# Kernel optimization log

Measured on AMD Instinct MI355X. Metric: run time of the kernel, lower is better.

## Reference

```python
import jax, jax.numpy as jnp
import numpy as np

B, S, D, H = 4, 2048, 1024, 16
DK = D // H


def setup_inputs() -> dict:
    key = jax.random.key(0)
    ks = jax.random.split(key, 9)
    sc = 1.0 / np.sqrt(D)
    return {
        "query": jax.random.normal(ks[0], (B, S, D), jnp.float32),
        "key": jax.random.normal(ks[1], (B, S, D), jnp.float32),
        "value": jax.random.normal(ks[2], (B, S, D), jnp.float32),
        "Wq": jax.random.normal(ks[3], (D, D), jnp.float32) * sc,
        "bq": jax.random.normal(ks[4], (D,), jnp.float32) * sc,
        "Wk": jax.random.normal(ks[5], (D, D), jnp.float32) * sc,
        "bk": jax.random.normal(ks[6], (D,), jnp.float32) * sc,
        "Wv": jax.random.normal(ks[7], (D, D), jnp.float32) * sc,
        "bv": jax.random.normal(ks[8], (D,), jnp.float32) * sc,
    }


def reference(query, key, value, Wq, bq, Wk, bk, Wv, bv):
    # QKV projections, split into heads: [B,S,D] -> [B,H,S,DK]
    q = (query @ Wq + bq).reshape(B, S, H, DK).transpose(0, 2, 1, 3)
    k = (key @ Wk + bk).reshape(B, S, H, DK).transpose(0, 2, 1, 3)
    v = (value @ Wv + bv).reshape(B, S, H, DK).transpose(0, 2, 1, 3)
    # NOTE: original module applies NO 1/sqrt(d_k) scaling
    attn = jnp.einsum("bhqd,bhkd->bhqk", q, k)
    attn = jax.nn.softmax(attn, axis=-1)  # dropout is identity at inference
    ctx = jnp.einsum("bhqk,bhkd->bhqd", attn, v)
    ctx = ctx.transpose(0, 2, 1, 3).reshape(B, S, D)
    # original adds residual to raw concatenated context (no output projection)
    return ctx + query
```

## Files before the change

### kernel.cpp

```cpp
#include <hip/hip_runtime.h>
#include <hip/hip_bf16.h>
#include <stdint.h>

#define Bb 4
#define Ss 2048
#define Dd 1024
#define Hh 16
#define DK 64
#define BH 64
#define Mm 8192
#define KVT 64

typedef __attribute__((ext_vector_type(8))) _Float16 f16x8;
typedef __attribute__((ext_vector_type(2))) _Float16 f16x2;
typedef __attribute__((ext_vector_type(4))) float f32x4;
typedef __attribute__((ext_vector_type(16))) float f32x16;
typedef __attribute__((ext_vector_type(2))) unsigned uint2v;

__device__ __forceinline__ void gload16(const _Float16* g, _Float16* lds) {
  __builtin_amdgcn_global_load_lds((const __attribute__((address_space(1))) unsigned int*)g,
                                   (__attribute__((address_space(3))) unsigned int*)lds, 16, 0, 0);
}

__device__ __forceinline__ unsigned pk2(float a, float b) {
  union { f16x2 h; unsigned u; } x;
  x.h[0] = (_Float16)a; x.h[1] = (_Float16)b;
  return x.u;
}

__global__ __launch_bounds__(256) void cvt_act(const float* __restrict__ q,
                                               const float* __restrict__ k,
                                               const float* __restrict__ v,
                                               _Float16* __restrict__ xq,
                                               _Float16* __restrict__ xk,
                                               _Float16* __restrict__ xv) {
  const float* src = blockIdx.z == 0 ? q : (blockIdx.z == 1 ? k : v);
  _Float16* dst = blockIdx.z == 0 ? xq : (blockIdx.z == 1 ? xk : xv);
  int i = (blockIdx.x * 256 + threadIdx.x) * 8;
  float4 a = *(const float4*)(src + i);
  float4 b = *(const float4*)(src + i + 4);
  union { f16x8 v8; _Float16 h[8]; } o;
  o.h[0] = (_Float16)a.x; o.h[1] = (_Float16)a.y; o.h[2] = (_Float16)a.z; o.h[3] = (_Float16)a.w;
  o.h[4] = (_Float16)b.x; o.h[5] = (_Float16)b.y; o.h[6] = (_Float16)b.z; o.h[7] = (_Float16)b.w;
  *(f16x8*)(dst + i) = o.v8;
}

__global__ __launch_bounds__(256) void cvt_wt(const float* __restrict__ wq,
                                              const float* __restrict__ wk,
                                              const float* __restrict__ wv,
                                              _Float16* __restrict__ tq,
                                              _Float16* __restrict__ tk,
                                              _Float16* __restrict__ tv) {
  const float* w = blockIdx.z == 0 ? wq : (blockIdx.z == 1 ? wk : wv);
  _Float16* o = blockIdx.z == 0 ? tq : (blockIdx.z == 1 ? tk : tv);
  __shared__ float tile[64][65];
  int k0 = blockIdx.x * 64;
  int n0 = blockIdx.y * 64;
  int t = threadIdx.x;
  int tr = t >> 4;
  int tc = (t & 15) * 4;
  for (int i = 0; i < 4; i++) {
    int r = i * 16 + tr;
    float4 val = *(const float4*)(w + (k0 + r) * Dd + n0 + tc);
    tile[r][tc + 0] = val.x; tile[r][tc + 1] = val.y;
    tile[r][tc + 2] = val.z; tile[r][tc + 3] = val.w;
  }
  __syncthreads();
  for (int i = 0; i < 2; i++) {
    int vdx = t + 256 * i;
    int rn = vdx >> 3;
    int c8 = (vdx & 7) * 8;
    union { f16x8 v8; _Float16 h[8]; } o2;
    for (int j = 0; j < 8; j++) o2.h[j] = (_Float16)tile[c8 + j][rn];
    *(f16x8*)(o + (n0 + rn) * Dd + k0 + c8) = o2.v8;
  }
}

__global__ __launch_bounds__(256) void gemm_qkv(
    const _Float16* __restrict__ xq, const _Float16* __restrict__ xk,
    const _Float16* __restrict__ xv,
    const _Float16* __restrict__ wtq, const _Float16* __restrict__ wtk,
    const _Float16* __restrict__ wtv,
    const float* __restrict__ bq, const float* __restrict__ bk, const float* __restrict__ bv,
    _Float16* __restrict__ oq, _Float16* __restrict__ ok,
    _Float16* __restrict__ ov) {
  int z = blockIdx.z;
  const _Float16* A  = z == 0 ? xq  : (z == 1 ? xk  : xv);
  const _Float16* Bt = z == 0 ? wtq : (z == 1 ? wtk : wtv);
  const float* bias  = z == 0 ? bq  : (z == 1 ? bk  : bv);
  _Float16* out      = z == 0 ? oq  : (z == 1 ? ok  : ov);

  __shared__ _Float16 As[128 * 64];
  __shared__ _Float16 Bs[128 * 64];

  int tid = threadIdx.x;
  int w = tid >> 6;
  int l = tid & 63;
  int lr = l & 15, lk = l >> 4;
  int m0 = blockIdx.x * 128;
  int n0 = blockIdx.y * 128;
  int wr = (w >> 1) * 64;
  int wc = (w & 1) * 64;

  f32x4 acc[4][4] = {};

  for (int kt = 0; kt < Dd; kt += 64) {
    __syncthreads();
    for (int i = 0; i < 4; i++) {
      int fbase = i * 256 + w * 64;
      int f = fbase + l;
      int r = f >> 3, c = (f & 7) * 8;
      gload16(A + (m0 + r) * Dd + kt + c, &As[fbase * 8]);
      gload16(Bt + (n0 + r) * Dd + kt + c, &Bs[fbase * 8]);
    }
    __syncthreads();
    for (int kh = 0; kh < 2; kh++) {
      f16x8 af[4], bfr[4];
      for (int mi = 0; mi < 4; mi++)
        af[mi] = *(const f16x8*)&As[(wr + mi * 16 + lr) * 64 + kh * 32 + lk * 8];
      for (int ni = 0; ni < 4; ni++)
        bfr[ni] = *(const f16x8*)&Bs[(wc + ni * 16 + lr) * 64 + kh * 32 + lk * 8];
      for (int mi = 0; mi < 4; mi++)
        for (int ni = 0; ni < 4; ni++)
          acc[mi][ni] = __builtin_amdgcn_mfma_f32_16x16x32_f16(af[mi], bfr[ni], acc[mi][ni], 0, 0, 0);
    }
  }

  for (int mi = 0; mi < 4; mi++) {
    for (int ni = 0; ni < 4; ni++) {
      int n = n0 + wc + ni * 16 + lr;
      float bval = bias[n];
      int h = n >> 6, dk = n & 63;
      for (int j = 0; j < 4; j++) {
        int m = m0 + wr + mi * 16 + lk * 4 + j;
        int b = m >> 11, s = m & 2047;
        out[((b * Hh + h) * Ss + s) * DK + dk] = (_Float16)(acc[mi][ni][j] + bval);
      }
    }
  }
}

__global__ __launch_bounds__(256) void transpose_v(const unsigned short* __restrict__ vin,
                                                   unsigned short* __restrict__ vout) {
  __shared__ unsigned short t[64][80];
  typedef __attribute__((ext_vector_type(8))) short s16x8;
  int bh = blockIdx.y;
  int s0 = blockIdx.x * 64;
  int tid = threadIdx.x;
  const unsigned short* vp = vin + bh * (Ss * DK);
  for (int i = 0; i < 2; i++) {
    int v = tid + 256 * i;
    int r = v >> 3, c8 = (v & 7) * 8;
    s16x8 val = *(const s16x8*)(vp + (s0 + r) * DK + c8);
    *(s16x8*)&t[r][c8] = val;
  }
  __syncthreads();
  unsigned short* op = vout + bh * (DK * Ss);
  for (int i = 0; i < 2; i++) {
    int v = tid + 256 * i;
    int rn = v >> 3;
    int c8 = (v & 7) * 8;
    union { s16x8 v8; unsigned short u[8]; } o2;
    for (int j = 0; j < 8; j++) o2.u[j] = t[c8 + j][rn];
    *(s16x8*)(op + rn * Ss + s0 + c8) = o2.v8;
  }
}

__global__ __launch_bounds__(256) void attn(const _Float16* __restrict__ Qb,
                                            const _Float16* __restrict__ Kb,
                                            const _Float16* __restrict__ Vt,
                                            const float* __restrict__ query,
                                            float* __restrict__ outp) {
  __shared__ _Float16 Kl[2][KVT * 64];
  __shared__ _Float16 Vl[2][KVT * 64];

  int tid = threadIdx.x;
  int w = tid >> 6, l = tid & 63;
  int l31 = l & 31, hi = l >> 5;
  int bh = blockIdx.x;
  int q0 = blockIdx.y * 128 + w * 32;
  const _Float16* Qp = Qb + bh * (Ss * DK);
  const _Float16* Kp = Kb + bh * (Ss * DK);
  const _Float16* Vp = Vt + bh * (DK * Ss);

  int srow = l >> 3;
  int sslot = (l & 7) ^ (srow & 7);
  int w16 = w * 16;
  const _Float16* ksrc0 = Kp + (w16 + srow) * DK + sslot * 8;
  const _Float16* ksrc1 = Kp + (w16 + 8 + srow) * DK + sslot * 8;
  const _Float16* vsrc0 = Vp + (w16 + srow) * Ss + sslot * 8;
  const _Float16* vsrc1 = Vp + (w16 + 8 + srow) * Ss + sslot * 8;

#define STAGE(KV0, BUF)                                                   \
  {                                                                       \
    gload16(ksrc0 + (KV0) * DK, &Kl[BUF][w16 * 64]);                      \
    gload16(ksrc1 + (KV0) * DK, &Kl[BUF][(w16 + 8) * 64]);                \
    gload16(vsrc0 + (KV0), &Vl[BUF][w16 * 64]);                           \
    gload16(vsrc1 + (KV0), &Vl[BUF][(w16 + 8) * 64]);                     \
  }

  f16x8 qf[4];
#pragma unroll
  for (int s = 0; s < 4; s++)
    qf[s] = *(const f16x8*)(Qp + (q0 + l31) * DK + s * 16 + hi * 8);

  f32x16 o0 = {}, o1 = {};
  float mrun = -1e30f, lrun = 0.f;

  int kv7 = l31 & 7;
  int rslot[4];
#pragma unroll
  for (int s = 0; s < 4; s++) rslot[s] = ((s * 2 + hi) ^ kv7) * 8;

  STAGE(0, 0)
  __syncthreads();

  int cur = 0;
  for (int kv0 = 0; kv0 < Ss; kv0 += KVT) {
    if (kv0 + KVT < Ss) STAGE(kv0 + KVT, cur ^ 1)

    const _Float16* Kc = &Kl[cur][0];
    f32x16 s0 = {}, s1 = {};
#pragma unroll
    for (int s = 0; s < 4; s++) {
      f16x8 ka = *(const f16x8*)&Kc[l31 * 64 + rslot[s]];
      s0 = __builtin_amdgcn_mfma_f32_32x32x16_f16(ka, qf[s], s0, 0, 0, 0);
    }
#pragma unroll
    for (int s = 0; s < 4; s++) {
      f16x8 kb = *(const f16x8*)&Kc[(32 + l31) * 64 + rslot[s]];
      s1 = __builtin_amdgcn_mfma_f32_32x32x16_f16(kb, qf[s], s1, 0, 0, 0);
    }

    float m8[8];
#pragma unroll
    for (int r = 0; r < 8; r++)
      m8[r] = fmaxf(fmaxf(s0[r], s0[r + 8]), fmaxf(s1[r], s1[r + 8]));
#pragma unroll
    for (int d = 4; d >= 1; d >>= 1)
#pragma unroll
      for (int r = 0; r < 4; r++) if (r < d) m8[r] = fmaxf(m8[r], m8[r + d]);
    float pm = fmaxf(m8[0], __shfl_xor(m8[0], 32));

    if (!__all(pm - mrun <= 8.f)) {
      float mn = fmaxf(mrun, pm);
      float sc_ = __expf(mrun - mn);
      mrun = mn;
      lrun *= sc_;
#pragma unroll
      for (int r = 0; r < 16; r++) { o0[r] *= sc_; o1[r] *= sc_; }
    }
#pragma unroll
    for (int r = 0; r < 16; r++) {
      s0[r] = __expf(s0[r] - mrun);
      s1[r] = __expf(s1[r] - mrun);
    }
    float sm[8];
#pragma unroll
    for (int r = 0; r < 8; r++) sm[r] = (s0[r] + s0[r + 8]) + (s1[r] + s1[r + 8]);
#pragma unroll
    for (int d = 4; d >= 1; d >>= 1)
#pragma unroll
      for (int r = 0; r < 4; r++) if (r < d) sm[r] += sm[r + d];
    lrun += sm[0] + __shfl_xor(sm[0], 32);

    const _Float16* Vc = &Vl[cur][0];
#define PVSTEP(SRC, OFF, KST)                                                   \
    {                                                                           \
      unsigned a0 = pk2(SRC[(OFF) + 0], SRC[(OFF) + 1]);                        \
      unsigned a1 = pk2(SRC[(OFF) + 2], SRC[(OFF) + 3]);                        \
      unsigned b0 = pk2(SRC[(OFF) + 4], SRC[(OFF) + 5]);                        \
      unsigned b1 = pk2(SRC[(OFF) + 6], SRC[(OFF) + 7]);                        \
      uint2v r0 = __builtin_amdgcn_permlane32_swap(a0, b0, false, false);       \
      uint2v r1 = __builtin_amdgcn_permlane32_swap(a1, b1, false, false);       \
      union { unsigned u[4]; f16x8 v; } pf;                                     \
      pf.u[0] = r0[0]; pf.u[1] = r1[0]; pf.u[2] = r0[1]; pf.u[3] = r1[1];       \
      f16x8 v0 = *(const f16x8*)&Vc[l31 * 64 + rslot[KST]];                     \
      f16x8 v1 = *(const f16x8*)&Vc[(32 + l31) * 64 + rslot[KST]];              \
      o0 = __builtin_amdgcn_mfma_f32_32x32x16_f16(v0, pf.v, o0, 0, 0, 0);       \
      o1 = __builtin_amdgcn_mfma_f32_32x32x16_f16(v1, pf.v, o1, 0, 0, 0);       \
    }
    PVSTEP(s0, 0, 0)
    PVSTEP(s0, 8, 1)
    PVSTEP(s1, 0, 2)
    PVSTEP(s1, 8, 3)
#undef PVSTEP

    __syncthreads();
    cur ^= 1;
  }

  int b = bh >> 4, h = bh & 15;
  float inv = 1.f / lrun;
  int base = (b * Ss + q0 + l31) * Dd + h * 64;
#pragma unroll
  for (int rq = 0; rq < 4; rq++) {
    int d0 = rq * 8 + hi * 4;
    float4 qv0 = *(const float4*)(query + base + d0);
    float4 ov0;
    ov0.x = o0[rq * 4 + 0] * inv + qv0.x;
    ov0.y = o0[rq * 4 + 1] * inv + qv0.y;
    ov0.z = o0[rq * 4 + 2] * inv + qv0.z;
    ov0.w = o0[rq * 4 + 3] * inv + qv0.w;
    *(float4*)(outp + base + d0) = ov0;
    float4 qv1 = *(const float4*)(query + base + 32 + d0);
    float4 ov1;
    ov1.x = o1[rq * 4 + 0] * inv + qv1.x;
    ov1.y = o1[rq * 4 + 1] * inv + qv1.y;
    ov1.z = o1[rq * 4 + 2] * inv + qv1.z;
    ov1.w = o1[rq * 4 + 3] * inv + qv1.w;
    *(float4*)(outp + base + 32 + d0) = ov1;
  }
#undef STAGE
}

extern "C" void kernel_launch(void* const* d_in, const int* in_sizes, int n_in,
                              void* d_out, int out_size, void* d_ws, size_t ws_size,
                              hipStream_t stream) {
  const float* query = (const float*)d_in[0];
  const float* key   = (const float*)d_in[1];
  const float* value = (const float*)d_in[2];
  const float* Wq = (const float*)d_in[3];
  const float* bq = (const float*)d_in[4];
  const float* Wk = (const float*)d_in[5];
  const float* bk = (const float*)d_in[6];
  const float* Wv = (const float*)d_in[7];
  const float* bv = (const float*)d_in[8];
  float* out = (float*)d_out;

  _Float16* ws = (_Float16*)d_ws;
  const size_t ACT = (size_t)Mm * Dd;
  const size_t WSZ = (size_t)Dd * Dd;
  _Float16* Xq   = ws;
  _Float16* Xk   = Xq + ACT;
  _Float16* Xv   = Xk + ACT;
  _Float16* Wtq  = Xv + ACT;
  _Float16* Wtk  = Wtq + WSZ;
  _Float16* Wtv  = Wtk + WSZ;
  _Float16* Qb   = Wtv + WSZ;
  _Float16* Kb   = Qb + ACT;
  _Float16* Vtmp = Kb + ACT;
  _Float16* VtT  = Vtmp + ACT;

  cvt_act<<<dim3(4096, 1, 3), dim3(256), 0, stream>>>(query, key, value, Xq, Xk, Xv);
  cvt_wt<<<dim3(16, 16, 3), dim3(256), 0, stream>>>(Wq, Wk, Wv, Wtq, Wtk, Wtv);
  gemm_qkv<<<dim3(64, 8, 3), dim3(256), 0, stream>>>(Xq, Xk, Xv, Wtq, Wtk, Wtv,
                                                     bq, bk, bv, Qb, Kb, Vtmp);
  transpose_v<<<dim3(32, 64), dim3(256), 0, stream>>>((const unsigned short*)Vtmp,
                                                      (unsigned short*)VtT);
  attn<<<dim3(64, 16), dim3(256), 0, stream>>>(Qb, Kb, VtT, query, out);
}
```

Baseline: 234.5 us.

## Fuse V transpose into GEMM epilogue, fold log2e into Wq, use exp2

The GEMM epilogue for V now writes the transposed [bh, dk, s] layout directly with 4-wide stores, so the separate transpose kernel and its extra pass over V are gone. Wq and bq are pre-scaled by log2(e) so softmax can use exp2f instead of __expf. The per-tile cross-lane shuffle for the row sum is deferred to a single shuffle after the loop, fp16 packing uses cvt_pkrtz, and s_setprio is raised around the MFMA blocks. Scaling Wq in fp16 changes rounding slightly, and cvt_pkrtz rounds toward zero rather than to nearest.

```diff
diff --git a/kernel.cpp b/kernel.cpp
--- a/kernel.cpp
+++ b/kernel.cpp
@@ -12,7 +12,8 @@
 #define KVT 64
 
 typedef __attribute__((ext_vector_type(8))) _Float16 f16x8;
-typedef __attribute__((ext_vector_type(2))) _Float16 f16x2;
+typedef __attribute__((ext_vector_type(4))) _Float16 f16x4;
+typedef __attribute__((ext_vector_type(2))) __fp16 fp16x2;
 typedef __attribute__((ext_vector_type(4))) float f32x4;
 typedef __attribute__((ext_vector_type(16))) float f32x16;
 typedef __attribute__((ext_vector_type(2))) unsigned uint2v;
@@ -22,9 +23,9 @@
                                    (__attribute__((address_space(3))) unsigned int*)lds, 16, 0, 0);
 }
 
-__device__ __forceinline__ unsigned pk2(float a, float b) {
-  union { f16x2 h; unsigned u; } x;
-  x.h[0] = (_Float16)a; x.h[1] = (_Float16)b;
+__device__ __forceinline__ unsigned pk2u(float a, float b) {
+  union { fp16x2 h; unsigned u; } x;
+  x.h = __builtin_amdgcn_cvt_pkrtz(a, b);
   return x.u;
 }
 
@@ -53,6 +54,7 @@
                                               _Float16* __restrict__ tv) {
   const float* w = blockIdx.z == 0 ? wq : (blockIdx.z == 1 ? wk : wv);
   _Float16* o = blockIdx.z == 0 ? tq : (blockIdx.z == 1 ? tk : tv);
+  float wscale = blockIdx.z == 0 ? 1.4426950408889634f : 1.0f;
   __shared__ float tile[64][65];
   int k0 = blockIdx.x * 64;
   int n0 = blockIdx.y * 64;
@@ -71,7 +73,7 @@
     int rn = vdx >> 3;
     int c8 = (vdx & 7) * 8;
     union { f16x8 v8; _Float16 h[8]; } o2;
-    for (int j = 0; j < 8; j++) o2.h[j] = (_Float16)tile[c8 + j][rn];
+    for (int j = 0; j < 8; j++) o2.h[j] = (_Float16)(tile[c8 + j][rn] * wscale);
     *(f16x8*)(o + (n0 + rn) * Dd + k0 + c8) = o2.v8;
   }
 }
@@ -89,6 +91,7 @@
   const _Float16* Bt = z == 0 ? wtq : (z == 1 ? wtk : wtv);
   const float* bias  = z == 0 ? bq  : (z == 1 ? bk  : bv);
   _Float16* out      = z == 0 ? oq  : (z == 1 ? ok  : ov);
+  float bscale       = z == 0 ? 1.4426950408889634f : 1.0f;
 
   __shared__ _Float16 As[128 * 64];
   __shared__ _Float16 Bs[128 * 64];
@@ -126,43 +129,32 @@
     }
   }
 
-  for (int mi = 0; mi < 4; mi++) {
-    for (int ni = 0; ni < 4; ni++) {
-      int n = n0 + wc + ni * 16 + lr;
-      float bval = bias[n];
-      int h = n >> 6, dk = n & 63;
-      for (int j = 0; j < 4; j++) {
-        int m = m0 + wr + mi * 16 + lk * 4 + j;
+  if (z == 2) {
+    for (int mi = 0; mi < 4; mi++) {
+      for (int ni = 0; ni < 4; ni++) {
+        int n = n0 + wc + ni * 16 + lr;
+        float bval = bias[n];
+        int h = n >> 6, dk = n & 63;
+        int m = m0 + wr + mi * 16 + lk * 4;
         int b = m >> 11, s = m & 2047;
-        out[((b * Hh + h) * Ss + s) * DK + dk] = (_Float16)(acc[mi][ni][j] + bval);
+        f16x4 o4;
+        for (int j = 0; j < 4; j++) o4[j] = (_Float16)(acc[mi][ni][j] + bval);
+        *(f16x4*)(out + ((size_t)((b * Hh + h) * DK + dk) * Ss + s)) = o4;
       }
     }
-  }
-}
-
-__global__ __launch_bounds__(256) void transpose_v(const unsigned short* __restrict__ vin,
-                                                   unsigned short* __restrict__ vout) {
-  __shared__ unsigned short t[64][80];
-  typedef __attribute__((ext_vector_type(8))) short s16x8;
-  int bh = blockIdx.y;
-  int s0 = blockIdx.x * 64;
-  int tid = threadIdx.x;
-  const unsigned short* vp = vin + bh * (Ss * DK);
-  for (int i = 0; i < 2; i++) {
-    int v = tid + 256 * i;
-    int r = v >> 3, c8 = (v & 7) * 8;
-    s16x8 val = *(const s16x8*)(vp + (s0 + r) * DK + c8);
-    *(s16x8*)&t[r][c8] = val;
-  }
-  __syncthreads();
-  unsigned short* op = vout + bh * (DK * Ss);
-  for (int i = 0; i < 2; i++) {
-    int v = tid + 256 * i;
-    int rn = v >> 3;
-    int c8 = (v & 7) * 8;
-    union { s16x8 v8; unsigned short u[8]; } o2;
-    for (int j = 0; j < 8; j++) o2.u[j] = t[c8 + j][rn];
-    *(s16x8*)(op + rn * Ss + s0 + c8) = o2.v8;
+  } else {
+    for (int mi = 0; mi < 4; mi++) {
+      for (int ni = 0; ni < 4; ni++) {
+        int n = n0 + wc + ni * 16 + lr;
+        float bval = bias[n] * bscale;
+        int h = n >> 6, dk = n & 63;
+        for (int j = 0; j < 4; j++) {
+          int m = m0 + wr + mi * 16 + lk * 4 + j;
+          int b = m >> 11, s = m & 2047;
+          out[((b * Hh + h) * Ss + s) * DK + dk] = (_Float16)(acc[mi][ni][j] + bval);
+        }
+      }
+    }
   }
 }
 
@@ -221,6 +213,7 @@
 
     const _Float16* Kc = &Kl[cur][0];
     f32x16 s0 = {}, s1 = {};
+    __builtin_amdgcn_s_setprio(1);
 #pragma unroll
     for (int s = 0; s < 4; s++) {
       f16x8 ka = *(const f16x8*)&Kc[l31 * 64 + rslot[s]];
@@ -231,6 +224,7 @@
       f16x8 kb = *(const f16x8*)&Kc[(32 + l31) * 64 + rslot[s]];
       s1 = __builtin_amdgcn_mfma_f32_32x32x16_f16(kb, qf[s], s1, 0, 0, 0);
     }
+    __builtin_amdgcn_s_setprio(0);
 
     float m8[8];
 #pragma unroll
@@ -244,7 +238,7 @@
 
     if (!__all(pm - mrun <= 8.f)) {
       float mn = fmaxf(mrun, pm);
-      float sc_ = __expf(mrun - mn);
+      float sc_ = exp2f(mrun - mn);
       mrun = mn;
       lrun *= sc_;
 #pragma unroll
@@ -252,25 +246,26 @@
     }
 #pragma unroll
     for (int r = 0; r < 16; r++) {
-      s0[r] = __expf(s0[r] - mrun);
-      s1[r] = __expf(s1[r] - mrun);
-    }
-    float sm[8];
-#pragma unroll
-    for (int r = 0; r < 8; r++) sm[r] = (s0[r] + s0[r + 8]) + (s1[r] + s1[r + 8]);
+      s0[r] = exp2f(s0[r] - mrun);
+      s1[r] = exp2f(s1[r] - mrun);
+    }
+    float s8[8];
+#pragma unroll
+    for (int r = 0; r < 8; r++) s8[r] = (s0[r] + s0[r + 8]) + (s1[r] + s1[r + 8]);
 #pragma unroll
     for (int d = 4; d >= 1; d >>= 1)
 #pragma unroll
-      for (int r = 0; r < 4; r++) if (r < d) sm[r] += sm[r + d];
-    lrun += sm[0] + __shfl_xor(sm[0], 32);
+      for (int r = 0; r < 4; r++) if (r < d) s8[r] += s8[r + d];
+    lrun += s8[0];
 
     const _Float16* Vc = &Vl[cur][0];
+    __builtin_amdgcn_s_setprio(1);
 #define PVSTEP(SRC, OFF, KST)                                                   \
     {                                                                           \
-      unsigned a0 = pk2(SRC[(OFF) + 0], SRC[(OFF) + 1]);                        \
-      unsigned a1 = pk2(SRC[(OFF) + 2], SRC[(OFF) + 3]);                        \
-      unsigned b0 = pk2(SRC[(OFF) + 4], SRC[(OFF) + 5]);                        \
-      unsigned b1 = pk2(SRC[(OFF) + 6], SRC[(OFF) + 7]);                        \
+      unsigned a0 = pk2u(SRC[(OFF) + 0], SRC[(OFF) + 1]);                       \
+      unsigned a1 = pk2u(SRC[(OFF) + 2], SRC[(OFF) + 3]);                       \
+      unsigned b0 = pk2u(SRC[(OFF) + 4], SRC[(OFF) + 5]);                       \
+      unsigned b1 = pk2u(SRC[(OFF) + 6], SRC[(OFF) + 7]);                       \
       uint2v r0 = __builtin_amdgcn_permlane32_swap(a0, b0, false, false);       \
       uint2v r1 = __builtin_amdgcn_permlane32_swap(a1, b1, false, false);       \
       union { unsigned u[4]; f16x8 v; } pf;                                     \
@@ -285,11 +280,13 @@
     PVSTEP(s1, 0, 2)
     PVSTEP(s1, 8, 3)
 #undef PVSTEP
+    __builtin_amdgcn_s_setprio(0);
 
     __syncthreads();
     cur ^= 1;
   }
 
+  lrun += __shfl_xor(lrun, 32);
   int b = bh >> 4, h = bh & 15;
   float inv = 1.f / lrun;
   int base = (b * Ss + q0 + l31) * Dd + h * 64;
@@ -339,14 +336,11 @@
   _Float16* Wtv  = Wtk + WSZ;
   _Float16* Qb   = Wtv + WSZ;
   _Float16* Kb   = Qb + ACT;
-  _Float16* Vtmp = Kb + ACT;
-  _Float16* VtT  = Vtmp + ACT;
+  _Float16* VtT  = Kb + ACT;
 
   cvt_act<<<dim3(4096, 1, 3), dim3(256), 0, stream>>>(query, key, value, Xq, Xk, Xv);
   cvt_wt<<<dim3(16, 16, 3), dim3(256), 0, stream>>>(Wq, Wk, Wv, Wtq, Wtk, Wtv);
   gemm_qkv<<<dim3(64, 8, 3), dim3(256), 0, stream>>>(Xq, Xk, Xv, Wtq, Wtk, Wtv,
-                                                     bq, bk, bv, Qb, Kb, Vtmp);
-  transpose_v<<<dim3(32, 64), dim3(256), 0, stream>>>((const unsigned short*)Vtmp,
-                                                      (unsigned short*)VtT);
+                                                     bq, bk, bv, Qb, Kb, VtT);
   attn<<<dim3(64, 16), dim3(256), 0, stream>>>(Qb, Kb, VtT, query, out);
 }
```

After: 250.4 us. 1.07x slower.
